# Performance work log

Measured on AMD Instinct MI355X. Metric: run time of the kernel, lower is better.

The kernel has to match this reference:

```python
import jax, jax.numpy as jnp
import numpy as np

N_NODES = 50000
N_EDGES = 600000
N_FEAT = 256
N_HID = 128
N_CLASS = 64
HEADS = 8
LEAKY_SLOPE = 0.2


def setup_inputs() -> dict:
    key = jax.random.key(0)
    ks = jax.random.split(key, 12)
    D0 = N_HID // HEADS  # 16 per-head dim, layer 0
    x = jax.random.normal(ks[0], (N_NODES, N_FEAT), dtype=jnp.float32)
    edge_index = jax.random.randint(ks[1], (2, N_EDGES), 0, N_NODES, dtype=jnp.int64)
    s0 = 1.0 / np.sqrt(N_FEAT)
    s1 = 1.0 / np.sqrt(N_HID)
    return {
        "x": x,
        "edge_index": edge_index,
        "W0": jax.random.normal(ks[2], (N_FEAT, HEADS * D0), dtype=jnp.float32) * s0,
        "a_src0": jax.random.normal(ks[3], (HEADS, D0), dtype=jnp.float32) * s0,
        "a_dst0": jax.random.normal(ks[4], (HEADS, D0), dtype=jnp.float32) * s0,
        "b0": jnp.zeros((HEADS * D0,), dtype=jnp.float32),
        "W1": jax.random.normal(ks[5], (N_HID, HEADS * N_CLASS), dtype=jnp.float32) * s1,
        "a_src1": jax.random.normal(ks[6], (HEADS, N_CLASS), dtype=jnp.float32) * s1,
        "a_dst1": jax.random.normal(ks[7], (HEADS, N_CLASS), dtype=jnp.float32) * s1,
        "b1": jnp.zeros((N_CLASS,), dtype=jnp.float32),
    }


def gat_conv(x, src, dst, W, a_s, a_d, b, concat, num_nodes):
    H, D = a_s.shape
    h = (x @ W).reshape(-1, H, D)                    # [N, H, D]
    alpha_s = jnp.einsum('nhd,hd->nh', h, a_s)       # [N, H]
    alpha_d = jnp.einsum('nhd,hd->nh', h, a_d)       # [N, H]
    e = jax.nn.leaky_relu(alpha_s[src] + alpha_d[dst], LEAKY_SLOPE)  # [E, H]
    # numerically stable edge-softmax grouped by destination node
    m = jax.ops.segment_max(e, dst, num_segments=num_nodes)
    m = jnp.where(jnp.isfinite(m), m, 0.0)           # nodes with no in-edges
    ex = jnp.exp(e - m[dst])
    denom = jax.ops.segment_sum(ex, dst, num_segments=num_nodes)
    alpha = ex / (denom[dst] + 1e-16)                # [E, H]
    msg = h[src] * alpha[:, :, None]                 # [E, H, D]
    out = jax.ops.segment_sum(msg, dst, num_segments=num_nodes)  # [N, H, D]
    if concat:
        out = out.reshape(num_nodes, H * D)
    else:
        out = out.mean(axis=1)
    return out + b


def reference(x, edge_index, W0, a_src0, a_dst0, b0, W1, a_src1, a_dst1, b1):
    src, dst = edge_index[0], edge_index[1]
    h = gat_conv(x, src, dst, W0, a_src0, a_dst0, b0, True, N_NODES)
    h = jax.nn.elu(h)  # eval mode: dropout is identity
    h = gat_conv(h, src, dst, W1, a_src1, a_dst1, b1, False, N_NODES)
    return jax.nn.log_softmax(h, axis=-1)
```

## Files before the change

### kernel.cpp

```cpp
#include <hip/hip_runtime.h>
#include <hip/hip_bf16.h>
#include <math.h>

#define NN 50000
#define NE 600000
#define NF 256
#define NHID 128
#define HEADS 8
#define D0 16
#define NCLS 64
#define NB1 196

#define PK0 (9 * 8 * 64 * 8)
#define PK1 (4 * 32 * 64 * 8)
#define PKA (4 * 64 * 8)
#define CASTN (NN * NF / 4)
#define PREPN (PK0 + PK1 + PKA)

typedef __attribute__((ext_vector_type(8))) short short8;
typedef __attribute__((ext_vector_type(4))) float floatx4;

__device__ __forceinline__ float bf16lo(uint v) { return __uint_as_float((v & 0xffffu) << 16); }
__device__ __forceinline__ float bf16hi(uint v) { return __uint_as_float(v & 0xffff0000u); }
__device__ __forceinline__ uint packbf16(float a, float b) {
    return (uint)__bfloat16_as_ushort(__float2bfloat16(a)) |
           ((uint)__bfloat16_as_ushort(__float2bfloat16(b)) << 16);
}
__device__ __forceinline__ short f2bf(float v) {
    return (short)__bfloat16_as_ushort(__float2bfloat16(v));
}
__device__ __forceinline__ float bf16tof(short v) {
    return __uint_as_float(((uint)(ushort)v) << 16);
}


__global__ void scan1_kernel(const int* __restrict__ deg, int* __restrict__ rs,
                             int* __restrict__ bsum) {
    __shared__ int sh[256];
    int tid = threadIdx.x;
    int i = blockIdx.x * 256 + tid;
    int v = (i < NN) ? deg[i] : 0;
    sh[tid] = v;
    __syncthreads();
    for (int off = 1; off < 256; off <<= 1) {
        int t = (tid >= off) ? sh[tid - off] : 0;
        __syncthreads();
        sh[tid] += t;
        __syncthreads();
    }
    if (i < NN) rs[i] = sh[tid] - v;
    if (tid == 255) bsum[blockIdx.x] = sh[255];
}

__global__ void scan2_kernel(const int* __restrict__ bsum, int* __restrict__ bsumx) {
    __shared__ int sh[256];
    int tid = threadIdx.x;
    int v = (tid < NB1) ? bsum[tid] : 0;
    sh[tid] = v;
    __syncthreads();
    for (int off = 1; off < 256; off <<= 1) {
        int t = (tid >= off) ? sh[tid - off] : 0;
        __syncthreads();
        sh[tid] += t;
        __syncthreads();
    }
    if (tid < NB1) bsumx[tid] = sh[tid] - v;
}

__global__ void scan3_kernel(int* __restrict__ rs, const int* __restrict__ bsumx) {
    int i = blockIdx.x * 256 + threadIdx.x;
    if (i < NN) rs[i] += bsumx[i >> 8];
}

__global__ void scatter_kernel(const int* __restrict__ ei, const int* __restrict__ rs,
                               int* __restrict__ cnt2, int* __restrict__ csr) {
    int e = blockIdx.x * 256 + threadIdx.x;
    if (e >= NE) return;
    int s = ei[e], d = ei[NE + e];
    int pos = rs[d] + atomicAdd(&cnt2[d], 1);
    csr[pos] = s;
}


__global__ void fused_prep_kernel(const float* __restrict__ x, short* __restrict__ xb,
                                  const int* __restrict__ ei, int* __restrict__ deg,
                                  const float* __restrict__ W0, const float* __restrict__ aS0,
                                  const float* __restrict__ aD0, const float* __restrict__ W1,
                                  const float* __restrict__ aS1, const float* __restrict__ aD1,
                                  short* __restrict__ Bp0, short* __restrict__ Bp1,
                                  short* __restrict__ wA1b) {
    int i = blockIdx.x * 256 + threadIdx.x;
    if (i < CASTN) {
        float4 v = ((const float4*)x)[i];
        short4 r;
        r.x = f2bf(v.x); r.y = f2bf(v.y); r.z = f2bf(v.z); r.w = f2bf(v.w);
        ((short4*)xb)[i] = r;
        return;
    }
    int e = i - CASTN;
    if (e < NE) {
        atomicAdd(&deg[ei[NE + e]], 1);
        return;
    }
    int tid = e - NE;
    if (tid < PK0) {
        int j = tid & 7, l = (tid >> 3) & 63, ks = (tid >> 9) & 7, t = tid >> 12;
        int k = ks * 32 + (l >> 4) * 8 + j;
        float v;
        if (t < 8) {
            int c = t * 16 + (l & 15);
            v = W0[(size_t)k * 128 + c];
        } else {
            int jj = l & 15;
            int hh = jj & 7;
            const float* av = (jj < 8) ? aS0 : aD0;
            float sum = 0.f;
            for (int dd = 0; dd < D0; ++dd)
                sum += W0[(size_t)k * 128 + hh * D0 + dd] * av[hh * D0 + dd];
            v = sum;
        }
        Bp0[tid] = f2bf(v);
    } else if (tid < PK0 + PK1) {
        int t2 = tid - PK0;
        int j = t2 & 7, l = (t2 >> 3) & 63, ks = (t2 >> 9) & 31, t = t2 >> 14;
        int kk = ks * 32 + (l >> 4) * 8 + j;
        int c = t * 16 + (l & 15);
        Bp1[t2] = f2bf(W1[(size_t)(kk & 127) * 512 + (kk >> 7) * 64 + c] * 0.125f);
    } else if (tid < PREPN) {
        int t3 = tid - PK0 - PK1;
        int j = t3 & 7, l = (t3 >> 3) & 63, ks = t3 >> 9;
        int k = ks * 32 + (l >> 4) * 8 + j;
        int c = l & 15;
        int h = c & 7;
        const float* av = (c < 8) ? aS1 : aD1;
        float sum = 0.f;
        for (int d2 = 0; d2 < NCLS; ++d2)
            sum += W1[(size_t)k * 512 + h * NCLS + d2] * av[h * NCLS + d2];
        wA1b[t3] = f2bf(sum);
    }
}


__global__ __launch_bounds__(256) void gemm0_mfma(const short* __restrict__ xb,
                                                  const short* __restrict__ Bp,
                                                  ushort* __restrict__ h0b,
                                                  float* __restrict__ as0,
                                                  float* __restrict__ ad0) {
    int lane = threadIdx.x & 63, wave = threadIdx.x >> 6;
    int rg = wave >> 1, cg = wave & 1;
    int q = lane >> 4, c16 = lane & 15;
    int row0 = blockIdx.x * 32 + rg * 16;
    int arow = row0 + c16;
    if (arow > NN - 1) arow = NN - 1;
    const short* ap = xb + (size_t)arow * NF + q * 8;
    floatx4 acc[5] = {};
#pragma unroll
    for (int ks = 0; ks < 8; ++ks) {
        short8 af = *(const short8*)(ap + ks * 32);
#pragma unroll
        for (int tt = 0; tt < 4; ++tt) {
            int t = cg * 4 + tt;
            short8 bf = *(const short8*)(Bp + (((size_t)t * 8 + ks) * 64 + lane) * 8);
            acc[tt] = __builtin_amdgcn_mfma_f32_16x16x32_bf16(af, bf, acc[tt], 0, 0, 0);
        }
        if (cg) {
            short8 bf = *(const short8*)(Bp + (((size_t)8 * 8 + ks) * 64 + lane) * 8);
            acc[4] = __builtin_amdgcn_mfma_f32_16x16x32_bf16(af, bf, acc[4], 0, 0, 0);
        }
    }
#pragma unroll
    for (int r = 0; r < 4; ++r) {
        int grow = row0 + q * 4 + r;
        if (grow >= NN) continue;
#pragma unroll
        for (int tt = 0; tt < 4; ++tt)
            h0b[(size_t)grow * NHID + cg * 64 + tt * 16 + c16] =
                (ushort)f2bf(acc[tt][r]);
        if (cg) {
            float v = acc[4][r];
            if (c16 < 8) as0[grow * 8 + c16] = v;
            else         ad0[grow * 8 + (c16 - 8)] = v;
        }
    }
}

__global__ __launch_bounds__(256) void alpha1_mfma(const ushort* __restrict__ x1b,
                                                   const short* __restrict__ wA1b,
                                                   float* __restrict__ as1,
                                                   float* __restrict__ ad1) {
    int lane = threadIdx.x & 63, wave = threadIdx.x >> 6;
    int q = lane >> 4, c16 = lane & 15;
    int row0 = blockIdx.x * 64 + wave * 16;
    int arow = row0 + c16;
    if (arow > NN - 1) arow = NN - 1;
    const short* ap = (const short*)x1b + (size_t)arow * NHID + q * 8;
    floatx4 acc = {};
#pragma unroll
    for (int ks = 0; ks < 4; ++ks) {
        short8 af = *(const short8*)(ap + ks * 32);
        short8 bf = *(const short8*)(wA1b + (((size_t)ks) * 64 + lane) * 8);
        acc = __builtin_amdgcn_mfma_f32_16x16x32_bf16(af, bf, acc, 0, 0, 0);
    }
#pragma unroll
    for (int r = 0; r < 4; ++r) {
        int grow = row0 + q * 4 + r;
        if (grow >= NN) continue;
        float v = acc[r];
        if (c16 < 8) as1[grow * 8 + c16] = v;
        else         ad1[grow * 8 + (c16 - 8)] = v;
    }
}


__global__ __launch_bounds__(256) void fused_edge0(
    const int* __restrict__ rs, const int* __restrict__ deg, const int* __restrict__ csr,
    const ushort* __restrict__ h0b, const float* __restrict__ as0, const float* __restrict__ ad0,
    const float* __restrict__ b0, ushort* __restrict__ x1b) {
    int d = (blockIdx.x * 256 + threadIdx.x) >> 6;
    int lane = threadIdx.x & 63;
    if (d >= NN) return;
    int row = rs[d], dg = deg[d];
    int hl = lane & 7, g = lane >> 3;
    int hp = lane >> 3;
    float adv = ad0[d * 8 + hl];
    float den = 0.f;
    float2 acc = {0.f, 0.f};
    for (int base = 0; base < dg; base += 8) {
        int i = base + g;
        int s = (i < dg) ? csr[row + i] : 0;
        float ev = as0[s * 8 + hl] + adv;
        ev = ev > 0.f ? ev : 0.2f * ev;
        float p = (i < dg) ? __expf(ev) : 0.f;
        den += p;
        uint vbuf[8];
#pragma unroll
        for (int g2 = 0; g2 < 8; ++g2) {
            int sg = __builtin_amdgcn_readlane(s, g2 * 8);
            vbuf[g2] = *(const uint*)(h0b + (size_t)sg * NHID + 2 * lane);
        }
#pragma unroll
        for (int g2 = 0; g2 < 8; ++g2) {
            float ph = __shfl(p, g2 * 8 + hp);
            acc.x += bf16lo(vbuf[g2]) * ph;
            acc.y += bf16hi(vbuf[g2]) * ph;
        }
    }
    den += __shfl_xor(den, 8);
    den += __shfl_xor(den, 16);
    den += __shfl_xor(den, 32);
    float dh = __shfl(den, hp);
    float inv = 1.f / (dh + 1e-16f);
    float2 bb = ((const float2*)b0)[lane];
    float o0 = acc.x * inv + bb.x;
    float o1 = acc.y * inv + bb.y;
    o0 = o0 > 0.f ? o0 : expf(o0) - 1.f;
    o1 = o1 > 0.f ? o1 : expf(o1) - 1.f;
    *(uint*)(x1b + (size_t)d * NHID + 2 * lane) = packbf16(o0, o1);
}

__global__ __launch_bounds__(256) void fused_edge1(
    const int* __restrict__ rs, const int* __restrict__ deg, const int* __restrict__ csr,
    const ushort* __restrict__ x1b, const float* __restrict__ as1, const float* __restrict__ ad1,
    const short* __restrict__ Bp1, const float* __restrict__ b1, float* __restrict__ out) {
    __shared__ ushort aggNsh[8][1032];
    __shared__ float Csh[4][8][64];
    int wave = threadIdx.x >> 6;
    int lane = threadIdx.x & 63;
    int gw = blockIdx.x * 4 + wave;
    int dA = 2 * gw;
    int dB = dA + 1;
    int q = lane >> 4, c16 = lane & 15, h7 = lane & 7;
    int d_l = (lane >= 32) ? dB : dA;
    int row_l = rs[d_l], dg_l = deg[d_l];
    bool V = ((lane & 8) == 0) == (lane < 32);
    float adv = ad1[d_l * 8 + h7];
    int dgA = __shfl(dg_l, 0);
    int dgB = __shfl(dg_l, 32);
    int dgmax = dgA > dgB ? dgA : dgB;
    float den = 0.f;
    floatx4 acc[8] = {};
    for (int base = 0; base < dgmax; base += 16) {
        short8 af;
        int sarr[8];
#pragma unroll
        for (int j = 0; j < 8; ++j) {
            int idx = base + (q & 1) * 8 + j;
            int s = 0;
            if (idx < dg_l) s = csr[row_l + idx];
            sarr[j] = s;
            float ev = as1[s * 8 + h7] + adv;
            ev = ev > 0.f ? ev : 0.2f * ev;
            float p = __expf(ev);
            p = (idx < dg_l && V) ? p : 0.f;
            short pb = f2bf(p);
            af[j] = pb;
            den += bf16tof(pb);
        }
#pragma unroll
        for (int t = 0; t < 8; ++t) {
            short8 bv;
#pragma unroll
            for (int j = 0; j < 8; ++j)
                bv[j] = (short)x1b[(size_t)sarr[j] * NHID + t * 16 + c16];
            acc[t] = __builtin_amdgcn_mfma_f32_16x16x32_bf16(af, bv, acc[t], 0, 0, 0);
        }
    }
    den += __shfl_xor(den, 8);
    den += __shfl_xor(den, 16);
    int hbase = (q & 1) * 4;
    int lrow = wave * 2 + (lane >> 5);
#pragma unroll
    for (int r = 0; r < 4; ++r) {
        int hh = hbase + r;
        float dh = __shfl(den, (lane & 32) + hh);
        float inv = 1.f / (dh + 1e-16f);
#pragma unroll
        for (int t = 0; t < 8; ++t)
            aggNsh[lrow][hh * 128 + t * 16 + c16] = (ushort)f2bf(acc[t][r] * inv);
    }
    __syncthreads();
    {
        floatx4 acc2[4] = {};
        const short* abase = (const short*)&aggNsh[c16 & 7][0];
        int ks0 = wave * 8;
#pragma unroll
        for (int kk = 0; kk < 8; ++kk) {
            int ks = ks0 + kk;
            short8 af2 = *(const short8*)(abase + ks * 32 + q * 8);
#pragma unroll
            for (int t = 0; t < 4; ++t) {
                short8 bf = *(const short8*)(Bp1 + (((size_t)t * 32 + ks) * 64 + lane) * 8);
                acc2[t] = __builtin_amdgcn_mfma_f32_16x16x32_bf16(af2, bf, acc2[t], 0, 0, 0);
            }
        }
        if (q < 2) {
#pragma unroll
            for (int r = 0; r < 4; ++r)
#pragma unroll
                for (int t = 0; t < 4; ++t)
                    Csh[wave][q * 4 + r][t * 16 + c16] = acc2[t][r];
        }
    }
    __syncthreads();
    float z0 = 0.f, z1 = 0.f;
#pragma unroll
    for (int w2 = 0; w2 < 4; ++w2) {
        z0 += Csh[w2][wave * 2][lane];
        z1 += Csh[w2][wave * 2 + 1][lane];
    }
    float bb = b1[lane];
    z0 += bb;
    z1 += bb;
    float mx0 = z0, mx1 = z1;
#pragma unroll
    for (int x = 1; x < 64; x <<= 1) {
        mx0 = fmaxf(mx0, __shfl_xor(mx0, x));
        mx1 = fmaxf(mx1, __shfl_xor(mx1, x));
    }
    float s0 = expf(z0 - mx0), s1 = expf(z1 - mx1);
#pragma unroll
    for (int x = 1; x < 64; x <<= 1) {
        s0 += __shfl_xor(s0, x);
        s1 += __shfl_xor(s1, x);
    }
    float lse0 = mx0 + logf(s0);
    float lse1 = mx1 + logf(s1);
    out[(size_t)dA * NCLS + lane] = z0 - lse0;
    out[(size_t)dB * NCLS + lane] = z1 - lse1;
}


extern "C" void kernel_launch(void* const* d_in, const int* in_sizes, int n_in,
                              void* d_out, int out_size, void* d_ws, size_t ws_size,
                              hipStream_t stream) {
    const float* x   = (const float*)d_in[0];
    const int*   ei  = (const int*)d_in[1];
    const float* W0  = (const float*)d_in[2];
    const float* aS0 = (const float*)d_in[3];
    const float* aD0 = (const float*)d_in[4];
    const float* b0  = (const float*)d_in[5];
    const float* W1  = (const float*)d_in[6];
    const float* aS1 = (const float*)d_in[7];
    const float* aD1 = (const float*)d_in[8];
    const float* b1  = (const float*)d_in[9];
    float* out = (float*)d_out;

    char* ws = (char*)d_ws;
    ushort* x1b = (ushort*)ws; ws += (size_t)NN * NHID * 2;
    ushort* h0b = (ushort*)ws; ws += (size_t)NN * NHID * 2;
    short* xb   = (short*)ws; ws += (size_t)NN * NF * 2;
    float* as0  = (float*)ws; ws += (size_t)NN * HEADS * 4;
    float* ad0  = (float*)ws; ws += (size_t)NN * HEADS * 4;
    float* as1  = (float*)ws; ws += (size_t)NN * HEADS * 4;
    float* ad1  = (float*)ws; ws += (size_t)NN * HEADS * 4;
    short* Bp0  = (short*)ws; ws += (size_t)PK0 * 2;
    short* Bp1  = (short*)ws; ws += (size_t)PK1 * 2;
    short* wA1b = (short*)ws; ws += (size_t)PKA * 2;
    int* deg    = (int*)ws; ws += (size_t)NN * 4;
    int* cnt2   = (int*)ws; ws += (size_t)NN * 4;
    int* rs     = (int*)ws; ws += (size_t)NN * 4;
    int* bsum   = (int*)ws; ws += 256 * 4;
    int* bsumx  = (int*)ws; ws += 256 * 4;
    int* csr    = (int*)ws; ws += (size_t)NE * 4;

    const int FUSEDN = CASTN + NE + PREPN;

    hipMemsetAsync(deg, 0, (size_t)2 * NN * 4, stream);
    fused_prep_kernel<<<(FUSEDN + 255) / 256, 256, 0, stream>>>(
        x, xb, ei, deg, W0, aS0, aD0, W1, aS1, aD1, Bp0, Bp1, wA1b);

    scan1_kernel<<<NB1, 256, 0, stream>>>(deg, rs, bsum);
    scan2_kernel<<<1, 256, 0, stream>>>(bsum, bsumx);
    scan3_kernel<<<NB1, 256, 0, stream>>>(rs, bsumx);
    scatter_kernel<<<(NE + 255) / 256, 256, 0, stream>>>(ei, rs, cnt2, csr);

    gemm0_mfma<<<(NN + 31) / 32, 256, 0, stream>>>(xb, Bp0, h0b, as0, ad0);
    fused_edge0<<<(NN + 3) / 4, 256, 0, stream>>>(rs, deg, csr, h0b, as0, ad0, b0, x1b);

    alpha1_mfma<<<(NN + 63) / 64, 256, 0, stream>>>(x1b, wA1b, as1, ad1);
    fused_edge1<<<NN / 8, 256, 0, stream>>>(rs, deg, csr, x1b, as1, ad1, Bp1, b1, out);
}
```

Measured before the change: 312.7 us.

## Unroll edge0 gather by two and widen edge1 blocks to sixteen nodes

In fused_edge0 the edge loop now handles 16 neighbours per iteration, so two batches of gather loads are in flight before any accumulation, which is meant to hide gather latency. fused_edge1 now uses 512-thread blocks covering 16 destination nodes. Its post-aggregation GEMM is repartitioned so each wave computes one 16-column output tile over half the K range, filling all 16 MFMA rows instead of 8 valid rows. This halves wasted MFMA work and halves the cross-wave reduction, but raises LDS use per block and register pressure, which may lower occupancy.

```diff
diff --git a/kernel.cpp b/kernel.cpp
--- a/kernel.cpp
+++ b/kernel.cpp
@@ -225,24 +225,39 @@
     float adv = ad0[d * 8 + hl];
     float den = 0.f;
     float2 acc = {0.f, 0.f};
-    for (int base = 0; base < dg; base += 8) {
-        int i = base + g;
-        int s = (i < dg) ? csr[row + i] : 0;
-        float ev = as0[s * 8 + hl] + adv;
-        ev = ev > 0.f ? ev : 0.2f * ev;
-        float p = (i < dg) ? __expf(ev) : 0.f;
-        den += p;
-        uint vbuf[8];
+    for (int base = 0; base < dg; base += 16) {
+        int i0 = base + g, i1 = base + 8 + g;
+        int s0 = (i0 < dg) ? csr[row + i0] : 0;
+        int s1 = (i1 < dg) ? csr[row + i1] : 0;
+        float ev0 = as0[s0 * 8 + hl] + adv;
+        ev0 = ev0 > 0.f ? ev0 : 0.2f * ev0;
+        float p0 = (i0 < dg) ? __expf(ev0) : 0.f;
+        float ev1 = as0[s1 * 8 + hl] + adv;
+        ev1 = ev1 > 0.f ? ev1 : 0.2f * ev1;
+        float p1 = (i1 < dg) ? __expf(ev1) : 0.f;
+        den += p0 + p1;
+        uint vbuf[16];
 #pragma unroll
         for (int g2 = 0; g2 < 8; ++g2) {
-            int sg = __builtin_amdgcn_readlane(s, g2 * 8);
+            int sg = __builtin_amdgcn_readlane(s0, g2 * 8);
             vbuf[g2] = *(const uint*)(h0b + (size_t)sg * NHID + 2 * lane);
         }
 #pragma unroll
         for (int g2 = 0; g2 < 8; ++g2) {
-            float ph = __shfl(p, g2 * 8 + hp);
+            int sg = __builtin_amdgcn_readlane(s1, g2 * 8);
+            vbuf[8 + g2] = *(const uint*)(h0b + (size_t)sg * NHID + 2 * lane);
+        }
+#pragma unroll
+        for (int g2 = 0; g2 < 8; ++g2) {
+            float ph = __shfl(p0, g2 * 8 + hp);
             acc.x += bf16lo(vbuf[g2]) * ph;
             acc.y += bf16hi(vbuf[g2]) * ph;
+        }
+#pragma unroll
+        for (int g2 = 0; g2 < 8; ++g2) {
+            float ph = __shfl(p1, g2 * 8 + hp);
+            acc.x += bf16lo(vbuf[8 + g2]) * ph;
+            acc.y += bf16hi(vbuf[8 + g2]) * ph;
         }
     }
     den += __shfl_xor(den, 8);
@@ -258,15 +273,15 @@
     *(uint*)(x1b + (size_t)d * NHID + 2 * lane) = packbf16(o0, o1);
 }
 
-__global__ __launch_bounds__(256) void fused_edge1(
+__global__ __launch_bounds__(512) void fused_edge1(
     const int* __restrict__ rs, const int* __restrict__ deg, const int* __restrict__ csr,
     const ushort* __restrict__ x1b, const float* __restrict__ as1, const float* __restrict__ ad1,
     const short* __restrict__ Bp1, const float* __restrict__ b1, float* __restrict__ out) {
-    __shared__ ushort aggNsh[8][1032];
-    __shared__ float Csh[4][8][64];
+    __shared__ ushort aggNsh[16][1036];
+    __shared__ float Csh[2][16][64];
     int wave = threadIdx.x >> 6;
     int lane = threadIdx.x & 63;
-    int gw = blockIdx.x * 4 + wave;
+    int gw = blockIdx.x * 8 + wave;
     int dA = 2 * gw;
     int dB = dA + 1;
     int q = lane >> 4, c16 = lane & 15, h7 = lane & 7;
@@ -320,34 +335,24 @@
     }
     __syncthreads();
     {
-        floatx4 acc2[4] = {};
-        const short* abase = (const short*)&aggNsh[c16 & 7][0];
-        int ks0 = wave * 8;
-#pragma unroll
-        for (int kk = 0; kk < 8; ++kk) {
+        int t = wave & 3;
+        int ks0 = (wave >> 2) * 16;
+        const short* abase = (const short*)&aggNsh[c16][0] + q * 8;
+        floatx4 acc2 = {};
+#pragma unroll
+        for (int kk = 0; kk < 16; ++kk) {
             int ks = ks0 + kk;
-            short8 af2 = *(const short8*)(abase + ks * 32 + q * 8);
-#pragma unroll
-            for (int t = 0; t < 4; ++t) {
-                short8 bf = *(const short8*)(Bp1 + (((size_t)t * 32 + ks) * 64 + lane) * 8);
-                acc2[t] = __builtin_amdgcn_mfma_f32_16x16x32_bf16(af2, bf, acc2[t], 0, 0, 0);
-            }
-        }
-        if (q < 2) {
-#pragma unroll
-            for (int r = 0; r < 4; ++r)
-#pragma unroll
-                for (int t = 0; t < 4; ++t)
-                    Csh[wave][q * 4 + r][t * 16 + c16] = acc2[t][r];
-        }
+            short8 af2 = *(const short8*)(abase + ks * 32);
+            short8 bf = *(const short8*)(Bp1 + (((size_t)t * 32 + ks) * 64 + lane) * 8);
+            acc2 = __builtin_amdgcn_mfma_f32_16x16x32_bf16(af2, bf, acc2, 0, 0, 0);
+        }
+#pragma unroll
+        for (int r = 0; r < 4; ++r)
+            Csh[wave >> 2][q * 4 + r][t * 16 + c16] = acc2[r];
     }
     __syncthreads();
-    float z0 = 0.f, z1 = 0.f;
-#pragma unroll
-    for (int w2 = 0; w2 < 4; ++w2) {
-        z0 += Csh[w2][wave * 2][lane];
-        z1 += Csh[w2][wave * 2 + 1][lane];
-    }
+    float z0 = Csh[0][wave * 2][lane] + Csh[1][wave * 2][lane];
+    float z1 = Csh[0][wave * 2 + 1][lane] + Csh[1][wave * 2 + 1][lane];
     float bb = b1[lane];
     z0 += bb;
     z1 += bb;
@@ -418,5 +423,5 @@
     fused_edge0<<<(NN + 3) / 4, 256, 0, stream>>>(rs, deg, csr, h0b, as0, ad0, b0, x1b);
 
     alpha1_mfma<<<(NN + 63) / 64, 256, 0, stream>>>(x1b, wA1b, as1, ad1);
-    fused_edge1<<<NN / 8, 256, 0, stream>>>(rs, deg, csr, x1b, as1, ad1, Bp1, b1, out);
-}
+    fused_edge1<<<NN / 16, 512, 0, stream>>>(rs, deg, csr, x1b, as1, ad1, Bp1, b1, out);
+}
```

New measurement: 336.4 us. 1.08x slower.
